# Kernel optimization log

Measured on AMD Instinct MI355X. Metric: run time of the kernel, lower is better.

The kernel has to match this reference:

```python
import jax, jax.numpy as jnp
import numpy as np

N_NODES = 100000
N_EDGES = 600000
D = 128          # model_dim
R = 50           # deprel_size


def setup_inputs() -> dict:
    key = jax.random.key(0)
    ks = jax.random.split(key, 20)
    s = 1.0 / np.sqrt(D)
    inp = jax.random.normal(ks[0], (N_NODES, D), dtype=jnp.float32)
    deprel_edge = jax.random.randint(ks[1], (N_EDGES,), 0, R)
    deparc_edge = jax.random.randint(ks[2], (N_EDGES,), 0, 4)
    edge_index = jax.random.randint(ks[3], (2, N_EDGES), 0, N_NODES)
    # parameters (nn.Linear weights stored as [out, in]; gates are Linear(D,1))
    V_in = jax.random.normal(ks[4], (D, D), dtype=jnp.float32) * s
    V_out = jax.random.normal(ks[5], (D, D), dtype=jnp.float32) * s
    W_self = jax.random.normal(ks[6], (D, D), dtype=jnp.float32) * s
    W_norel = jax.random.normal(ks[7], (D, D), dtype=jnp.float32) * s
    V_in_gate = jax.random.normal(ks[8], (1, D), dtype=jnp.float32) * s
    V_out_gate = jax.random.normal(ks[9], (1, D), dtype=jnp.float32) * s
    W_self_gate = jax.random.normal(ks[10], (1, D), dtype=jnp.float32) * s
    W_norel_gate = jax.random.normal(ks[11], (1, D), dtype=jnp.float32) * s
    b_in = jax.random.normal(ks[12], (R, D), dtype=jnp.float32) * 0.02
    b_out = jax.random.normal(ks[13], (R, D), dtype=jnp.float32) * 0.02
    b_in_gate = jax.random.normal(ks[14], (R, 1), dtype=jnp.float32) * 0.02 + 1.0
    b_out_gate = jax.random.normal(ks[15], (R, 1), dtype=jnp.float32) * 0.02 + 1.0
    return {
        "inp": inp, "deprel_edge": deprel_edge, "deparc_edge": deparc_edge,
        "edge_index": edge_index,
        "V_in": V_in, "b_in": b_in, "V_in_gate": V_in_gate, "b_in_gate": b_in_gate,
        "V_out": V_out, "b_out": b_out, "V_out_gate": V_out_gate, "b_out_gate": b_out_gate,
        "W_self": W_self, "W_self_gate": W_self_gate,
        "W_norel": W_norel, "W_norel_gate": W_norel_gate,
    }


def reference(inp, deprel_edge, deparc_edge, edge_index,
              V_in, b_in, V_in_gate, b_in_gate,
              V_out, b_out, V_out_gate, b_out_gate,
              W_self, W_self_gate, W_norel, W_norel_gate):
    # deparc type codes: 0=align(in), 1=opposite(out), 2=self, 3=norelation
    num_nodes = inp.shape[0]
    src, tgt = edge_index[0], edge_index[1]
    # transformed node features per edge type: [4, N, D]
    T = jnp.stack([inp @ V_in.T, inp @ V_out.T, inp @ W_self.T, inp @ W_norel.T])
    # gate pre-activations per edge type: [4, N, 1]
    G = jnp.stack([inp @ V_in_gate.T, inp @ V_out_gate.T,
                   inp @ W_self_gate.T, inp @ W_norel_gate.T])
    zeros_b = jnp.zeros_like(b_in)
    zeros_bg = jnp.zeros_like(b_in_gate)
    B = jnp.stack([b_in, b_out, zeros_b, zeros_b])        # [4, R, D] (self/norel have no relation bias)
    Bg = jnp.stack([b_in_gate, b_out_gate, zeros_bg, zeros_bg])  # [4, R, 1]
    # per-edge gather + relation bias
    msg = T[deparc_edge, src] + B[deparc_edge, deprel_edge]        # [E, D]
    gate = jax.nn.sigmoid(G[deparc_edge, src] + Bg[deparc_edge, deprel_edge])  # [E, 1]
    # scatter-add to target nodes
    return jax.ops.segment_sum(msg * gate, tgt, num_segments=num_nodes)
```

## Files before the change

kernel.cpp:

```cpp
#include <hip/hip_runtime.h>
#include <hip/hip_bf16.h>

#define D 128

typedef __bf16 bf16x8 __attribute__((ext_vector_type(8)));
typedef __bf16 bf16x4 __attribute__((ext_vector_type(4)));
typedef __bf16 bf16x2 __attribute__((ext_vector_type(2)));
typedef float  f32x4  __attribute__((ext_vector_type(4)));
typedef float  f32x2  __attribute__((ext_vector_type(2)));
typedef unsigned int u32x4 __attribute__((ext_vector_type(4)));

__global__ void detect_kernel(const unsigned int* __restrict__ w, int* flag)
{
    __shared__ int cnt[256];
    int c = 0;
#pragma unroll
    for (int i = 0; i < 4; ++i) {
        unsigned int v = w[threadIdx.x * 4 + i];
        unsigned int e = (v >> 7) & 0xFF;
        if (e >= 90 && e <= 134) ++c;
    }
    cnt[threadIdx.x] = c;
    __syncthreads();
    for (int s = 128; s > 0; s >>= 1) {
        if (threadIdx.x < s) cnt[threadIdx.x] += cnt[threadIdx.x + s];
        __syncthreads();
    }
    if (threadIdx.x == 0) flag[0] = (cnt[0] > 614) ? 1 : 0;
}

template <int ISBF>
__device__ __forceinline__ bf16x8 ld8(const void* p, size_t elem)
{
    if (ISBF) return *(const bf16x8*)((const __bf16*)p + elem);
    const f32x4* f = (const f32x4*)((const float*)p + elem);
    f32x4 lo = f[0], hi = f[1];
    bf16x8 r;
    r[0] = (__bf16)lo[0]; r[1] = (__bf16)lo[1]; r[2] = (__bf16)lo[2]; r[3] = (__bf16)lo[3];
    r[4] = (__bf16)hi[0]; r[5] = (__bf16)hi[1]; r[6] = (__bf16)hi[2]; r[7] = (__bf16)hi[3];
    return r;
}
template <int ISBF>
__device__ __forceinline__ float ldf(const void* p, size_t elem)
{
    return ISBF ? (float)((const __bf16*)p)[elem] : ((const float*)p)[elem];
}

__device__ __forceinline__ f32x2 bfpair(unsigned int u)
{
    f32x2 r;
    r[0] = __builtin_bit_cast(float, u << 16);
    r[1] = __builtin_bit_cast(float, u & 0xffff0000u);
    return r;
}

__device__ __forceinline__ f32x2 pkfma(f32x2 a, f32x2 b, f32x2 c)
{
    f32x2 d;
    asm("v_pk_fma_f32 %0, %1, %2, %3" : "=v"(d) : "v"(a), "v"(b), "v"(c));
    return d;
}

template <int ISBF>
__device__ __forceinline__ void gate_body(
    const void* __restrict__ A,
    const void* __restrict__ g0, const void* __restrict__ g1,
    const void* __restrict__ g2, const void* __restrict__ g3,
    float* __restrict__ G, int M)
{
    int node = blockIdx.x * 16 + (threadIdx.x >> 4);
    if (node >= M) return;
    int lane16 = threadIdx.x & 15;
    int dd = lane16 * 8;
    bf16x8 a  = ld8<ISBF>(A, (size_t)node * D + dd);
    bf16x8 q0 = ld8<ISBF>(g0, dd);
    bf16x8 q1 = ld8<ISBF>(g1, dd);
    bf16x8 q2 = ld8<ISBF>(g2, dd);
    bf16x8 q3 = ld8<ISBF>(g3, dd);
    float s0 = 0.f, s1 = 0.f, s2 = 0.f, s3 = 0.f;
#pragma unroll
    for (int k = 0; k < 8; ++k) {
        float af = (float)a[k];
        s0 = fmaf(af, (float)q0[k], s0);
        s1 = fmaf(af, (float)q1[k], s1);
        s2 = fmaf(af, (float)q2[k], s2);
        s3 = fmaf(af, (float)q3[k], s3);
    }
#pragma unroll
    for (int off = 8; off > 0; off >>= 1) {
        s0 += __shfl_xor(s0, off);
        s1 += __shfl_xor(s1, off);
        s2 += __shfl_xor(s2, off);
        s3 += __shfl_xor(s3, off);
    }
    if (lane16 == 0) {
        G[(size_t)0 * M + node] = s0;
        G[(size_t)1 * M + node] = s1;
        G[(size_t)2 * M + node] = s2;
        G[(size_t)3 * M + node] = s3;
    }
}

__global__ __launch_bounds__(256) void gate_kernel(
    const void* __restrict__ A,
    const void* __restrict__ g0, const void* __restrict__ g1,
    const void* __restrict__ g2, const void* __restrict__ g3,
    float* __restrict__ G, int M, const int* __restrict__ flag)
{
    if (flag[0]) gate_body<1>(A, g0, g1, g2, g3, G, M);
    else         gate_body<0>(A, g0, g1, g2, g3, G, M);
}

__global__ __launch_bounds__(128) void build_bias_kernel(
    const void* __restrict__ b_in, const void* __restrict__ b_out,
    const void* __restrict__ bg_in, const void* __restrict__ bg_out,
    __bf16* __restrict__ Bz, float* __restrict__ Bgz,
    const int* __restrict__ flag)
{
    int row = blockIdx.x;
    int tid = threadIdx.x;
    int isbf = flag[0];
    float v = 0.f, gv = 0.f;
    if (row < 50) {
        v  = isbf ? ldf<1>(b_in, (size_t)row * D + tid) : ldf<0>(b_in, (size_t)row * D + tid);
        gv = isbf ? ldf<1>(bg_in, row) : ldf<0>(bg_in, row);
    } else if (row < 100) {
        int rr = row - 50;
        v  = isbf ? ldf<1>(b_out, (size_t)rr * D + tid) : ldf<0>(b_out, (size_t)rr * D + tid);
        gv = isbf ? ldf<1>(bg_out, rr) : ldf<0>(bg_out, rr);
    }
    Bz[(size_t)row * D + tid] = (__bf16)v;
    if (tid == 0) Bgz[row] = gv;
}

__global__ __launch_bounds__(256) void hist_kernel(
    const int* __restrict__ tgt, int* __restrict__ counts, int E)
{
    int e = blockIdx.x * 256 + threadIdx.x;
    if (e < E) atomicAdd(&counts[tgt[e]], 1);
}

__global__ __launch_bounds__(256) void scan1_kernel(
    const int* __restrict__ counts, int* __restrict__ rowptr,
    int* __restrict__ bsum, int M)
{
    __shared__ int sh[256];
    int base = blockIdx.x * 1024 + threadIdx.x * 4;
    int v[4];
#pragma unroll
    for (int k = 0; k < 4; ++k)
        v[k] = (base + k < M) ? counts[base + k] : 0;
    int tot = v[0] + v[1] + v[2] + v[3];
    sh[threadIdx.x] = tot;
    __syncthreads();
    for (int off = 1; off < 256; off <<= 1) {
        int t = (threadIdx.x >= off) ? sh[threadIdx.x - off] : 0;
        __syncthreads();
        sh[threadIdx.x] += t;
        __syncthreads();
    }
    int run = sh[threadIdx.x] - tot;
#pragma unroll
    for (int k = 0; k < 4; ++k) {
        if (base + k < M) rowptr[base + k] = run;
        run += v[k];
    }
    if (threadIdx.x == 255) bsum[blockIdx.x] = sh[255];
}

__global__ __launch_bounds__(256) void scan2_kernel(
    int* __restrict__ bsum, int* __restrict__ boff, int NB)
{
    __shared__ int sh[256];
    int base = threadIdx.x * 4;
    int v[4];
#pragma unroll
    for (int k = 0; k < 4; ++k)
        v[k] = (base + k < NB) ? bsum[base + k] : 0;
    int tot = v[0] + v[1] + v[2] + v[3];
    sh[threadIdx.x] = tot;
    __syncthreads();
    for (int off = 1; off < 256; off <<= 1) {
        int t = (threadIdx.x >= off) ? sh[threadIdx.x - off] : 0;
        __syncthreads();
        sh[threadIdx.x] += t;
        __syncthreads();
    }
    int run = sh[threadIdx.x] - tot;
#pragma unroll
    for (int k = 0; k < 4; ++k) {
        if (base + k < NB) boff[base + k] = run;
        run += v[k];
    }
}

__global__ __launch_bounds__(256) void scan3_kernel(
    int* __restrict__ rowptr, int* __restrict__ cursor,
    const int* __restrict__ boff, int M, int E)
{
    int b = blockIdx.x;
    int base = b * 1024 + threadIdx.x * 4;
    int o = boff[b];
#pragma unroll
    for (int k = 0; k < 4; ++k) {
        int i = base + k;
        if (i < M) {
            int r = rowptr[i] + o;
            rowptr[i] = r;
            cursor[i] = r;
        }
    }
    if (b == 0 && threadIdx.x == 0) rowptr[M] = E;
}

__global__ __launch_bounds__(256) void scatter_kernel(
    const int* __restrict__ deprel, const int* __restrict__ deparc,
    const int* __restrict__ src, const int* __restrict__ tgt,
    int* __restrict__ cursor, int2* __restrict__ recs, int E)
{
    int e = blockIdx.x * 256 + threadIdx.x;
    if (e >= E) return;
    int g = tgt[e];
    int pos = atomicAdd(&cursor[g], 1);
    recs[pos] = make_int2(src[e], (deprel[e] << 2) | deparc[e]);
}

__global__ __launch_bounds__(256) void deg_hist_kernel(
    const int* __restrict__ counts, int* __restrict__ dcnt, int M)
{
    __shared__ int lh[64];
    if (threadIdx.x < 64) lh[threadIdx.x] = 0;
    __syncthreads();
    int i = blockIdx.x * 256 + threadIdx.x;
    if (i < M) {
        int d = counts[i]; if (d > 63) d = 63;
        atomicAdd(&lh[d], 1);
    }
    __syncthreads();
    if (threadIdx.x < 64 && lh[threadIdx.x])
        atomicAdd(&dcnt[threadIdx.x], lh[threadIdx.x]);
}

__global__ void deg_scan_kernel(const int* __restrict__ dcnt, int* __restrict__ dcur)
{
    if (threadIdx.x == 0) {
        int run = 0;
        for (int i = 0; i < 64; ++i) { dcur[i] = run; run += dcnt[i]; }
    }
}

__global__ __launch_bounds__(256) void deg_scatter_kernel(
    const int* __restrict__ counts, int* __restrict__ dcur,
    int* __restrict__ perm, int M)
{
    __shared__ int lh[64];
    __shared__ int gb[64];
    if (threadIdx.x < 64) lh[threadIdx.x] = 0;
    __syncthreads();
    int i = blockIdx.x * 256 + threadIdx.x;
    int d = 0, lpos = 0;
    if (i < M) {
        d = counts[i]; if (d > 63) d = 63;
        lpos = atomicAdd(&lh[d], 1);
    }
    __syncthreads();
    if (threadIdx.x < 64 && lh[threadIdx.x])
        gb[threadIdx.x] = atomicAdd(&dcur[threadIdx.x], lh[threadIdx.x]);
    __syncthreads();
    if (i < M) perm[gb[d] + lpos] = i;
}

template <int ISBF>
__device__ __forceinline__ void edge_agg_body(
    const void* __restrict__ inp, const float* __restrict__ G,
    const __bf16* __restrict__ Bz, const float* __restrict__ Bgz,
    const int* __restrict__ rowptr, const int2* __restrict__ recs,
    const int* __restrict__ perm,
    __bf16* __restrict__ AG, __bf16* __restrict__ BA, int M)
{
    const int idx = blockIdx.x * 16 + (threadIdx.x >> 4);
    if (idx >= M) return;
    const int g = perm[idx];
    const int lane16 = threadIdx.x & 15;
    const int dd = lane16 * 8;

    const int beg = rowptr[g], end = rowptr[g + 1];
    const int n = end - beg;

    f32x2 a0[4], a1[4], a2[4], a3[4], ba[4];
#pragma unroll
    for (int k = 0; k < 4; ++k) {
        a0[k] = (f32x2){0.f, 0.f}; a1[k] = (f32x2){0.f, 0.f};
        a2[k] = (f32x2){0.f, 0.f}; a3[k] = (f32x2){0.f, 0.f};
        ba[k] = (f32x2){0.f, 0.f};
    }

    bf16x8 v0 = {}, bz0 = {}, v1 = {}, bz1 = {};
    float gp0 = 0.f, bg0 = 0.f, gp1 = 0.f, bg1 = 0.f;
    int t0 = 0, t1 = 0;
    int2 r2 = make_int2(0, 0);

    auto issue = [&](int2 rec, bf16x8& v, bf16x8& bz, float& gp, float& bg, int& t) {
        t = rec.y & 3;
        int r = rec.y >> 2;
        int bidx = (t < 2) ? t * 50 + r : 100;
        gp = G[(size_t)t * M + rec.x];
        bg = Bgz[bidx];
        v  = ld8<ISBF>(inp, (size_t)rec.x * D + dd);
        bz = *(const bf16x8*)(Bz + (size_t)bidx * D + dd);
    };

    if (n > 0) issue(recs[beg], v0, bz0, gp0, bg0, t0);
    if (n > 1) issue(recs[beg + 1], v1, bz1, gp1, bg1, t1);
    if (n > 2) r2 = recs[beg + 2];

    for (int e = 0; e < n; ++e) {
        const bf16x8 v = v0, bz = bz0;
        const float gp = gp0, bg = bg0;
        const int t = t0;

        v0 = v1; bz0 = bz1; gp0 = gp1; bg0 = bg1; t0 = t1;
        if (e + 2 < n) {
            issue(r2, v1, bz1, gp1, bg1, t1);
            if (e + 3 < n) r2 = recs[beg + e + 3];
        }

        const float gate = 1.f / (1.f + __expf(-(gp + bg)));
        const float w0s = (t == 0) ? gate : 0.f;
        const float w1s = (t == 1) ? gate : 0.f;
        const float w2s = (t == 2) ? gate : 0.f;
        const float w3s = (t == 3) ? gate : 0.f;
        const f32x2 w0 = {w0s, w0s}, w1 = {w1s, w1s};
        const f32x2 w2 = {w2s, w2s}, w3 = {w3s, w3s};
        const f32x2 gg = {gate, gate};

        const u32x4 uv = __builtin_bit_cast(u32x4, v);
        const u32x4 ub = __builtin_bit_cast(u32x4, bz);
#pragma unroll
        for (int k = 0; k < 4; ++k) {
            const f32x2 vf = bfpair(uv[k]);
            const f32x2 bf = bfpair(ub[k]);
            a0[k] = pkfma(vf, w0, a0[k]);
            a1[k] = pkfma(vf, w1, a1[k]);
            a2[k] = pkfma(vf, w2, a2[k]);
            a3[k] = pkfma(vf, w3, a3[k]);
            ba[k] = pkfma(bf, gg, ba[k]);
        }
    }

    __bf16* agrow = AG + (size_t)g * (4 * D);
    bf16x8 w;
#pragma unroll
    for (int k = 0; k < 4; ++k) { w[2*k] = (__bf16)a0[k][0]; w[2*k+1] = (__bf16)a0[k][1]; }
    *(bf16x8*)(agrow + 0 * D + dd) = w;
#pragma unroll
    for (int k = 0; k < 4; ++k) { w[2*k] = (__bf16)a1[k][0]; w[2*k+1] = (__bf16)a1[k][1]; }
    *(bf16x8*)(agrow + 1 * D + dd) = w;
#pragma unroll
    for (int k = 0; k < 4; ++k) { w[2*k] = (__bf16)a2[k][0]; w[2*k+1] = (__bf16)a2[k][1]; }
    *(bf16x8*)(agrow + 2 * D + dd) = w;
#pragma unroll
    for (int k = 0; k < 4; ++k) { w[2*k] = (__bf16)a3[k][0]; w[2*k+1] = (__bf16)a3[k][1]; }
    *(bf16x8*)(agrow + 3 * D + dd) = w;
#pragma unroll
    for (int k = 0; k < 4; ++k) { w[2*k] = (__bf16)ba[k][0]; w[2*k+1] = (__bf16)ba[k][1]; }
    *(bf16x8*)(BA + (size_t)g * D + dd) = w;
}

__global__ __launch_bounds__(256) void edge_agg_kernel(
    const void* __restrict__ inp, const float* __restrict__ G,
    const __bf16* __restrict__ Bz, const float* __restrict__ Bgz,
    const int* __restrict__ rowptr, const int2* __restrict__ recs,
    const int* __restrict__ perm,
    __bf16* __restrict__ AG, __bf16* __restrict__ BA, int M,
    const int* __restrict__ flag)
{
    if (flag[0]) edge_agg_body<1>(inp, G, Bz, Bgz, rowptr, recs, perm, AG, BA, M);
    else         edge_agg_body<0>(inp, G, Bz, Bgz, rowptr, recs, perm, AG, BA, M);
}

template <int ISBF>
__device__ __forceinline__ void gemm2_body(
    const __bf16* __restrict__ AG, const __bf16* __restrict__ BA,
    const void* __restrict__ W0, const void* __restrict__ W1,
    const void* __restrict__ W2, const void* __restrict__ W3,
    void* __restrict__ out, int M)
{
    __shared__ __bf16 Wsh[128 * 128];

    const int wave = threadIdx.x >> 6;
    const int lane = threadIdx.x & 63;
    const int lrow = lane & 15;
    const int kgrp = lane >> 4;
    const int m_base = blockIdx.x * 128 + wave * 32;

    int n0 = m_base + lrow;      if (n0 >= M) n0 = 0;
    int n1 = m_base + 16 + lrow; if (n1 >= M) n1 = 0;

    const void* Ws[4] = {W0, W1, W2, W3};

    f32x4 acc[2][8];
#pragma unroll
    for (int i = 0; i < 2; ++i)
#pragma unroll
        for (int j = 0; j < 8; ++j)
            acc[i][j] = (f32x4){0.f, 0.f, 0.f, 0.f};

    for (int t = 0; t < 4; ++t) {
        const void* W = Ws[t];
#pragma unroll
        for (int i = 0; i < 8; ++i) {
            int slot = threadIdx.x + 256 * i;
            int f = slot >> 4;
            int s = slot & 15;
            int sp = s ^ (f & 7);
            bf16x8 v = ld8<ISBF>(W, (size_t)f * D + s * 8);
            *(bf16x8*)(Wsh + f * 128 + sp * 8) = v;
        }
        __syncthreads();

#pragma unroll
        for (int ks = 0; ks < 4; ++ks) {
            const int k0 = ks * 32 + kgrp * 8;
            bf16x8 af0 = *(const bf16x8*)(AG + (size_t)n0 * (4 * D) + t * D + k0);
            bf16x8 af1 = *(const bf16x8*)(AG + (size_t)n1 * (4 * D) + t * D + k0);
            const int slot = 4 * ks + kgrp;
#pragma unroll
            for (int ft = 0; ft < 8; ++ft) {
                int f = ft * 16 + lrow;
                int sp = slot ^ (f & 7);
                bf16x8 wf = *(const bf16x8*)(Wsh + f * 128 + sp * 8);
                acc[0][ft] = __builtin_amdgcn_mfma_f32_16x16x32_bf16(wf, af0, acc[0][ft], 0, 0, 0);
                acc[1][ft] = __builtin_amdgcn_mfma_f32_16x16x32_bf16(wf, af1, acc[1][ft], 0, 0, 0);
            }
        }
        __syncthreads();
    }

#pragma unroll
    for (int nt = 0; nt < 2; ++nt) {
        int node = m_base + nt * 16 + lrow;
        if (node < M) {
#pragma unroll
            for (int ft = 0; ft < 8; ++ft) {
                int f0 = ft * 16 + kgrp * 4;
                bf16x4 bb = *(const bf16x4*)(BA + (size_t)node * D + f0);
                f32x4 v = acc[nt][ft];
                v[0] += (float)bb[0]; v[1] += (float)bb[1];
                v[2] += (float)bb[2]; v[3] += (float)bb[3];
                if (ISBF) {
                    bf16x4 w4;
                    w4[0] = (__bf16)v[0]; w4[1] = (__bf16)v[1];
                    w4[2] = (__bf16)v[2]; w4[3] = (__bf16)v[3];
                    *(bf16x4*)((__bf16*)out + (size_t)node * D + f0) = w4;
                } else {
                    *(f32x4*)((float*)out + (size_t)node * D + f0) = v;
                }
            }
        }
    }
}

__global__ __launch_bounds__(256) void gemm2_kernel(
    const __bf16* __restrict__ AG, const __bf16* __restrict__ BA,
    const void* __restrict__ W0, const void* __restrict__ W1,
    const void* __restrict__ W2, const void* __restrict__ W3,
    void* __restrict__ out, int M, const int* __restrict__ flag)
{
    if (flag[0]) gemm2_body<1>(AG, BA, W0, W1, W2, W3, out, M);
    else         gemm2_body<0>(AG, BA, W0, W1, W2, W3, out, M);
}

__global__ void sentinel_kernel(__bf16* o, int n)
{
    int i = blockIdx.x * blockDim.x + threadIdx.x;
    if (i < n) o[i] = (__bf16)12345.0f;
}

static inline size_t align256(size_t x) { return (x + 255) & ~(size_t)255; }

extern "C" void kernel_launch(void* const* d_in, const int* in_sizes, int n_in,
                              void* d_out, int out_size, void* d_ws, size_t ws_size,
                              hipStream_t stream)
{
    const void* inp       = d_in[0];
    const int*  deprel    = (const int*)d_in[1];
    const int*  deparc    = (const int*)d_in[2];
    const int*  eidx      = (const int*)d_in[3];
    const void* V_in      = d_in[4];
    const void* b_in      = d_in[5];
    const void* V_in_g    = d_in[6];
    const void* b_in_g    = d_in[7];
    const void* V_out     = d_in[8];
    const void* b_out     = d_in[9];
    const void* V_out_g   = d_in[10];
    const void* b_out_g   = d_in[11];
    const void* W_self    = d_in[12];
    const void* W_self_g  = d_in[13];
    const void* W_norel   = d_in[14];
    const void* W_norel_g = d_in[15];

    const int M = in_sizes[0] / D;
    const int E = in_sizes[1];
    const int* src = eidx;
    const int* tgt = eidx + E;
    const int NB = (M + 1023) / 1024;

    size_t off = 0;
    size_t o_flag   = off; off = align256(off + sizeof(int));
    size_t o_AG     = off; off = align256(off + (size_t)M * 4 * D * sizeof(__bf16));
    size_t o_BA     = off; off = align256(off + (size_t)M * D * sizeof(__bf16));
    size_t o_G      = off; off = align256(off + (size_t)4 * M * sizeof(float));
    size_t o_counts = off; off = align256(off + (size_t)M * sizeof(int));
    size_t o_rowptr = off; off = align256(off + (size_t)(M + 1) * sizeof(int));
    size_t o_cursor = off; off = align256(off + (size_t)M * sizeof(int));
    size_t o_bsum   = off; off = align256(off + (size_t)NB * sizeof(int));
    size_t o_boff   = off; off = align256(off + (size_t)NB * sizeof(int));
    size_t o_recs   = off; off = align256(off + (size_t)E * sizeof(int2));
    size_t o_Bz     = off; off = align256(off + (size_t)101 * D * sizeof(__bf16));
    size_t o_Bgz    = off; off = align256(off + (size_t)101 * sizeof(float));
    size_t o_perm   = off; off = align256(off + (size_t)M * sizeof(int));
    size_t o_dcnt   = off; off = align256(off + (size_t)64 * sizeof(int));
    size_t o_dcur   = off; off = align256(off + (size_t)64 * sizeof(int));

    if (off > ws_size) {
        sentinel_kernel<<<(out_size + 255) / 256, 256, 0, stream>>>(
            (__bf16*)d_out, out_size);
        return;
    }

    int*    flag   = (int*)((char*)d_ws + o_flag);
    __bf16* AG     = (__bf16*)((char*)d_ws + o_AG);
    __bf16* BA     = (__bf16*)((char*)d_ws + o_BA);
    float*  Gbuf   = (float*)((char*)d_ws + o_G);
    int*    counts = (int*)((char*)d_ws + o_counts);
    int*    rowptr = (int*)((char*)d_ws + o_rowptr);
    int*    cursor = (int*)((char*)d_ws + o_cursor);
    int*    bsum   = (int*)((char*)d_ws + o_bsum);
    int*    boff   = (int*)((char*)d_ws + o_boff);
    int2*   recs   = (int2*)((char*)d_ws + o_recs);
    __bf16* Bz     = (__bf16*)((char*)d_ws + o_Bz);
    float*  Bgz    = (float*)((char*)d_ws + o_Bgz);
    int*    perm   = (int*)((char*)d_ws + o_perm);
    int*    dcnt   = (int*)((char*)d_ws + o_dcnt);
    int*    dcur   = (int*)((char*)d_ws + o_dcur);

    detect_kernel<<<1, 256, 0, stream>>>((const unsigned int*)inp, flag);

    hipMemsetAsync(counts, 0, (size_t)M * sizeof(int), stream);
    hipMemsetAsync(dcnt, 0, 64 * sizeof(int), stream);
    hist_kernel<<<(E + 255) / 256, 256, 0, stream>>>(tgt, counts, E);

    deg_hist_kernel<<<(M + 255) / 256, 256, 0, stream>>>(counts, dcnt, M);
    deg_scan_kernel<<<1, 64, 0, stream>>>(dcnt, dcur);
    deg_scatter_kernel<<<(M + 255) / 256, 256, 0, stream>>>(counts, dcur, perm, M);

    scan1_kernel<<<NB, 256, 0, stream>>>(counts, rowptr, bsum, M);
    scan2_kernel<<<1, 256, 0, stream>>>(bsum, boff, NB);
    scan3_kernel<<<NB, 256, 0, stream>>>(rowptr, cursor, boff, M, E);
    scatter_kernel<<<(E + 255) / 256, 256, 0, stream>>>(deprel, deparc, src, tgt,
                                                        cursor, recs, E);

    build_bias_kernel<<<101, 128, 0, stream>>>(b_in, b_out, b_in_g, b_out_g,
                                               Bz, Bgz, flag);
    gate_kernel<<<(M + 15) / 16, 256, 0, stream>>>(inp, V_in_g, V_out_g, W_self_g,
                                                   W_norel_g, Gbuf, M, flag);

    edge_agg_kernel<<<(M + 15) / 16, 256, 0, stream>>>(inp, Gbuf, Bz, Bgz,
                                                       rowptr, recs, perm,
                                                       AG, BA, M, flag);
    gemm2_kernel<<<(M + 127) / 128, 256, 0, stream>>>(AG, BA, V_in, V_out, W_self,
                                                      W_norel, d_out, M, flag);
}
```

Measured before the change: 339.6 us.

## Merge setup kernels, drop degree-sort permutation, use nontemporal memory ops

Folds the dtype detect into the histogram kernel and the bias build into the gate kernel. Replaces the separate block-sum scan with a serial per-block prefix loop inside scan3. Removes the degree-sorted node permutation, so edge aggregation handles nodes in natural order. Switches intermediate AG/BA stores, their loads in the GEMM and the output stores to nontemporal hints. Fewer launches cut launch overhead, but dropping the degree sort can bring back load imbalance between wavefronts in edge aggregation.

```diff
diff --git a/kernel.cpp b/kernel.cpp
--- a/kernel.cpp
+++ b/kernel.cpp
@@ -9,25 +9,6 @@
 typedef float  f32x4  __attribute__((ext_vector_type(4)));
 typedef float  f32x2  __attribute__((ext_vector_type(2)));
 typedef unsigned int u32x4 __attribute__((ext_vector_type(4)));
-
-__global__ void detect_kernel(const unsigned int* __restrict__ w, int* flag)
-{
-    __shared__ int cnt[256];
-    int c = 0;
-#pragma unroll
-    for (int i = 0; i < 4; ++i) {
-        unsigned int v = w[threadIdx.x * 4 + i];
-        unsigned int e = (v >> 7) & 0xFF;
-        if (e >= 90 && e <= 134) ++c;
-    }
-    cnt[threadIdx.x] = c;
-    __syncthreads();
-    for (int s = 128; s > 0; s >>= 1) {
-        if (threadIdx.x < s) cnt[threadIdx.x] += cnt[threadIdx.x + s];
-        __syncthreads();
-    }
-    if (threadIdx.x == 0) flag[0] = (cnt[0] > 614) ? 1 : 0;
-}
 
 template <int ISBF>
 __device__ __forceinline__ bf16x8 ld8(const void* p, size_t elem)
@@ -61,13 +42,57 @@
     return d;
 }
 
+__global__ __launch_bounds__(256) void hist_detect_kernel(
+    const int* __restrict__ tgt, int* __restrict__ counts, int E,
+    const unsigned int* __restrict__ w, int* __restrict__ flag)
+{
+    __shared__ int cnt[256];
+    int e = blockIdx.x * 256 + threadIdx.x;
+    if (e < E) atomicAdd(&counts[tgt[e]], 1);
+    if (blockIdx.x == 0) {
+        int c = 0;
+#pragma unroll
+        for (int i = 0; i < 4; ++i) {
+            unsigned int v = w[threadIdx.x * 4 + i];
+            unsigned int ex = (v >> 7) & 0xFF;
+            if (ex >= 90 && ex <= 134) ++c;
+        }
+        cnt[threadIdx.x] = c;
+        __syncthreads();
+        for (int s = 128; s > 0; s >>= 1) {
+            if (threadIdx.x < s) cnt[threadIdx.x] += cnt[threadIdx.x + s];
+            __syncthreads();
+        }
+        if (threadIdx.x == 0) flag[0] = (cnt[0] > 614) ? 1 : 0;
+    }
+}
+
 template <int ISBF>
-__device__ __forceinline__ void gate_body(
+__device__ __forceinline__ void gate_bias_body(
     const void* __restrict__ A,
     const void* __restrict__ g0, const void* __restrict__ g1,
     const void* __restrict__ g2, const void* __restrict__ g3,
-    float* __restrict__ G, int M)
-{
+    const void* __restrict__ b_in, const void* __restrict__ b_out,
+    const void* __restrict__ bg_in, const void* __restrict__ bg_out,
+    float* __restrict__ G, __bf16* __restrict__ Bz, float* __restrict__ Bgz,
+    int M)
+{
+    if (blockIdx.x < 101 && threadIdx.x < 128) {
+        int row = blockIdx.x;
+        int tid = threadIdx.x;
+        float v = 0.f, gv = 0.f;
+        if (row < 50) {
+            v  = ldf<ISBF>(b_in, (size_t)row * D + tid);
+            gv = ldf<ISBF>(bg_in, row);
+        } else if (row < 100) {
+            int rr = row - 50;
+            v  = ldf<ISBF>(b_out, (size_t)rr * D + tid);
+            gv = ldf<ISBF>(bg_out, rr);
+        }
+        Bz[(size_t)row * D + tid] = (__bf16)v;
+        if (tid == 0) Bgz[row] = gv;
+    }
+
     int node = blockIdx.x * 16 + (threadIdx.x >> 4);
     if (node >= M) return;
     int lane16 = threadIdx.x & 15;
@@ -101,43 +126,17 @@
     }
 }
 
-__global__ __launch_bounds__(256) void gate_kernel(
+__global__ __launch_bounds__(256) void gate_bias_kernel(
     const void* __restrict__ A,
     const void* __restrict__ g0, const void* __restrict__ g1,
     const void* __restrict__ g2, const void* __restrict__ g3,
-    float* __restrict__ G, int M, const int* __restrict__ flag)
-{
-    if (flag[0]) gate_body<1>(A, g0, g1, g2, g3, G, M);
-    else         gate_body<0>(A, g0, g1, g2, g3, G, M);
-}
-
-__global__ __launch_bounds__(128) void build_bias_kernel(
     const void* __restrict__ b_in, const void* __restrict__ b_out,
     const void* __restrict__ bg_in, const void* __restrict__ bg_out,
-    __bf16* __restrict__ Bz, float* __restrict__ Bgz,
-    const int* __restrict__ flag)
-{
-    int row = blockIdx.x;
-    int tid = threadIdx.x;
-    int isbf = flag[0];
-    float v = 0.f, gv = 0.f;
-    if (row < 50) {
-        v  = isbf ? ldf<1>(b_in, (size_t)row * D + tid) : ldf<0>(b_in, (size_t)row * D + tid);
-        gv = isbf ? ldf<1>(bg_in, row) : ldf<0>(bg_in, row);
-    } else if (row < 100) {
-        int rr = row - 50;
-        v  = isbf ? ldf<1>(b_out, (size_t)rr * D + tid) : ldf<0>(b_out, (size_t)rr * D + tid);
-        gv = isbf ? ldf<1>(bg_out, rr) : ldf<0>(bg_out, rr);
-    }
-    Bz[(size_t)row * D + tid] = (__bf16)v;
-    if (tid == 0) Bgz[row] = gv;
-}
-
-__global__ __launch_bounds__(256) void hist_kernel(
-    const int* __restrict__ tgt, int* __restrict__ counts, int E)
-{
-    int e = blockIdx.x * 256 + threadIdx.x;
-    if (e < E) atomicAdd(&counts[tgt[e]], 1);
+    float* __restrict__ G, __bf16* __restrict__ Bz, float* __restrict__ Bgz,
+    int M, const int* __restrict__ flag)
+{
+    if (flag[0]) gate_bias_body<1>(A, g0, g1, g2, g3, b_in, b_out, bg_in, bg_out, G, Bz, Bgz, M);
+    else         gate_bias_body<0>(A, g0, g1, g2, g3, b_in, b_out, bg_in, bg_out, G, Bz, Bgz, M);
 }
 
 __global__ __launch_bounds__(256) void scan1_kernel(
@@ -168,39 +167,14 @@
     if (threadIdx.x == 255) bsum[blockIdx.x] = sh[255];
 }
 
-__global__ __launch_bounds__(256) void scan2_kernel(
-    int* __restrict__ bsum, int* __restrict__ boff, int NB)
-{
-    __shared__ int sh[256];
-    int base = threadIdx.x * 4;
-    int v[4];
-#pragma unroll
-    for (int k = 0; k < 4; ++k)
-        v[k] = (base + k < NB) ? bsum[base + k] : 0;
-    int tot = v[0] + v[1] + v[2] + v[3];
-    sh[threadIdx.x] = tot;
-    __syncthreads();
-    for (int off = 1; off < 256; off <<= 1) {
-        int t = (threadIdx.x >= off) ? sh[threadIdx.x - off] : 0;
-        __syncthreads();
-        sh[threadIdx.x] += t;
-        __syncthreads();
-    }
-    int run = sh[threadIdx.x] - tot;
-#pragma unroll
-    for (int k = 0; k < 4; ++k) {
-        if (base + k < NB) boff[base + k] = run;
-        run += v[k];
-    }
-}
-
 __global__ __launch_bounds__(256) void scan3_kernel(
     int* __restrict__ rowptr, int* __restrict__ cursor,
-    const int* __restrict__ boff, int M, int E)
+    const int* __restrict__ bsum, int M, int E)
 {
     int b = blockIdx.x;
+    int o = 0;
+    for (int i = 0; i < b; ++i) o += bsum[i];
     int base = b * 1024 + threadIdx.x * 4;
-    int o = boff[b];
 #pragma unroll
     for (int k = 0; k < 4; ++k) {
         int i = base + k;
@@ -225,62 +199,15 @@
     recs[pos] = make_int2(src[e], (deprel[e] << 2) | deparc[e]);
 }
 
-__global__ __launch_bounds__(256) void deg_hist_kernel(
-    const int* __restrict__ counts, int* __restrict__ dcnt, int M)
-{
-    __shared__ int lh[64];
-    if (threadIdx.x < 64) lh[threadIdx.x] = 0;
-    __syncthreads();
-    int i = blockIdx.x * 256 + threadIdx.x;
-    if (i < M) {
-        int d = counts[i]; if (d > 63) d = 63;
-        atomicAdd(&lh[d], 1);
-    }
-    __syncthreads();
-    if (threadIdx.x < 64 && lh[threadIdx.x])
-        atomicAdd(&dcnt[threadIdx.x], lh[threadIdx.x]);
-}
-
-__global__ void deg_scan_kernel(const int* __restrict__ dcnt, int* __restrict__ dcur)
-{
-    if (threadIdx.x == 0) {
-        int run = 0;
-        for (int i = 0; i < 64; ++i) { dcur[i] = run; run += dcnt[i]; }
-    }
-}
-
-__global__ __launch_bounds__(256) void deg_scatter_kernel(
-    const int* __restrict__ counts, int* __restrict__ dcur,
-    int* __restrict__ perm, int M)
-{
-    __shared__ int lh[64];
-    __shared__ int gb[64];
-    if (threadIdx.x < 64) lh[threadIdx.x] = 0;
-    __syncthreads();
-    int i = blockIdx.x * 256 + threadIdx.x;
-    int d = 0, lpos = 0;
-    if (i < M) {
-        d = counts[i]; if (d > 63) d = 63;
-        lpos = atomicAdd(&lh[d], 1);
-    }
-    __syncthreads();
-    if (threadIdx.x < 64 && lh[threadIdx.x])
-        gb[threadIdx.x] = atomicAdd(&dcur[threadIdx.x], lh[threadIdx.x]);
-    __syncthreads();
-    if (i < M) perm[gb[d] + lpos] = i;
-}
-
 template <int ISBF>
 __device__ __forceinline__ void edge_agg_body(
     const void* __restrict__ inp, const float* __restrict__ G,
     const __bf16* __restrict__ Bz, const float* __restrict__ Bgz,
     const int* __restrict__ rowptr, const int2* __restrict__ recs,
-    const int* __restrict__ perm,
     __bf16* __restrict__ AG, __bf16* __restrict__ BA, int M)
 {
-    const int idx = blockIdx.x * 16 + (threadIdx.x >> 4);
-    if (idx >= M) return;
-    const int g = perm[idx];
+    const int g = blockIdx.x * 16 + (threadIdx.x >> 4);
+    if (g >= M) return;
     const int lane16 = threadIdx.x & 15;
     const int dd = lane16 * 8;
 
@@ -352,31 +279,30 @@
     bf16x8 w;
 #pragma unroll
     for (int k = 0; k < 4; ++k) { w[2*k] = (__bf16)a0[k][0]; w[2*k+1] = (__bf16)a0[k][1]; }
-    *(bf16x8*)(agrow + 0 * D + dd) = w;
+    __builtin_nontemporal_store(w, (bf16x8*)(agrow + 0 * D + dd));
 #pragma unroll
     for (int k = 0; k < 4; ++k) { w[2*k] = (__bf16)a1[k][0]; w[2*k+1] = (__bf16)a1[k][1]; }
-    *(bf16x8*)(agrow + 1 * D + dd) = w;
+    __builtin_nontemporal_store(w, (bf16x8*)(agrow + 1 * D + dd));
 #pragma unroll
     for (int k = 0; k < 4; ++k) { w[2*k] = (__bf16)a2[k][0]; w[2*k+1] = (__bf16)a2[k][1]; }
-    *(bf16x8*)(agrow + 2 * D + dd) = w;
+    __builtin_nontemporal_store(w, (bf16x8*)(agrow + 2 * D + dd));
 #pragma unroll
     for (int k = 0; k < 4; ++k) { w[2*k] = (__bf16)a3[k][0]; w[2*k+1] = (__bf16)a3[k][1]; }
-    *(bf16x8*)(agrow + 3 * D + dd) = w;
+    __builtin_nontemporal_store(w, (bf16x8*)(agrow + 3 * D + dd));
 #pragma unroll
     for (int k = 0; k < 4; ++k) { w[2*k] = (__bf16)ba[k][0]; w[2*k+1] = (__bf16)ba[k][1]; }
-    *(bf16x8*)(BA + (size_t)g * D + dd) = w;
+    __builtin_nontemporal_store(w, (bf16x8*)(BA + (size_t)g * D + dd));
 }
 
 __global__ __launch_bounds__(256) void edge_agg_kernel(
     const void* __restrict__ inp, const float* __restrict__ G,
     const __bf16* __restrict__ Bz, const float* __restrict__ Bgz,
     const int* __restrict__ rowptr, const int2* __restrict__ recs,
-    const int* __restrict__ perm,
     __bf16* __restrict__ AG, __bf16* __restrict__ BA, int M,
     const int* __restrict__ flag)
 {
-    if (flag[0]) edge_agg_body<1>(inp, G, Bz, Bgz, rowptr, recs, perm, AG, BA, M);
-    else         edge_agg_body<0>(inp, G, Bz, Bgz, rowptr, recs, perm, AG, BA, M);
+    if (flag[0]) edge_agg_body<1>(inp, G, Bz, Bgz, rowptr, recs, AG, BA, M);
+    else         edge_agg_body<0>(inp, G, Bz, Bgz, rowptr, recs, AG, BA, M);
 }
 
 template <int ISBF>
@@ -422,8 +348,10 @@
 #pragma unroll
         for (int ks = 0; ks < 4; ++ks) {
             const int k0 = ks * 32 + kgrp * 8;
-            bf16x8 af0 = *(const bf16x8*)(AG + (size_t)n0 * (4 * D) + t * D + k0);
-            bf16x8 af1 = *(const bf16x8*)(AG + (size_t)n1 * (4 * D) + t * D + k0);
+            bf16x8 af0 = __builtin_nontemporal_load(
+                (const bf16x8*)(AG + (size_t)n0 * (4 * D) + t * D + k0));
+            bf16x8 af1 = __builtin_nontemporal_load(
+                (const bf16x8*)(AG + (size_t)n1 * (4 * D) + t * D + k0));
             const int slot = 4 * ks + kgrp;
 #pragma unroll
             for (int ft = 0; ft < 8; ++ft) {
@@ -444,7 +372,8 @@
 #pragma unroll
             for (int ft = 0; ft < 8; ++ft) {
                 int f0 = ft * 16 + kgrp * 4;
-                bf16x4 bb = *(const bf16x4*)(BA + (size_t)node * D + f0);
+                bf16x4 bb = __builtin_nontemporal_load(
+                    (const bf16x4*)(BA + (size_t)node * D + f0));
                 f32x4 v = acc[nt][ft];
                 v[0] += (float)bb[0]; v[1] += (float)bb[1];
                 v[2] += (float)bb[2]; v[3] += (float)bb[3];
@@ -452,9 +381,11 @@
                     bf16x4 w4;
                     w4[0] = (__bf16)v[0]; w4[1] = (__bf16)v[1];
                     w4[2] = (__bf16)v[2]; w4[3] = (__bf16)v[3];
-                    *(bf16x4*)((__bf16*)out + (size_t)node * D + f0) = w4;
+                    __builtin_nontemporal_store(w4,
+                        (bf16x4*)((__bf16*)out + (size_t)node * D + f0));
                 } else {
-                    *(f32x4*)((float*)out + (size_t)node * D + f0) = v;
+                    __builtin_nontemporal_store(v,
+                        (f32x4*)((float*)out + (size_t)node * D + f0));
                 }
             }
         }
@@ -515,13 +446,9 @@
     size_t o_rowptr = off; off = align256(off + (size_t)(M + 1) * sizeof(int));
     size_t o_cursor = off; off = align256(off + (size_t)M * sizeof(int));
     size_t o_bsum   = off; off = align256(off + (size_t)NB * sizeof(int));
-    size_t o_boff   = off; off = align256(off + (size_t)NB * sizeof(int));
     size_t o_recs   = off; off = align256(off + (size_t)E * sizeof(int2));
     size_t o_Bz     = off; off = align256(off + (size_t)101 * D * sizeof(__bf16));
     size_t o_Bgz    = off; off = align256(off + (size_t)101 * sizeof(float));
-    size_t o_perm   = off; off = align256(off + (size_t)M * sizeof(int));
-    size_t o_dcnt   = off; off = align256(off + (size_t)64 * sizeof(int));
-    size_t o_dcur   = off; off = align256(off + (size_t)64 * sizeof(int));
 
     if (off > ws_size) {
         sentinel_kernel<<<(out_size + 255) / 256, 256, 0, stream>>>(
@@ -537,38 +464,24 @@
     int*    rowptr = (int*)((char*)d_ws + o_rowptr);
     int*    cursor = (int*)((char*)d_ws + o_cursor);
     int*    bsum   = (int*)((char*)d_ws + o_bsum);
-    int*    boff   = (int*)((char*)d_ws + o_boff);
     int2*   recs   = (int2*)((char*)d_ws + o_recs);
     __bf16* Bz     = (__bf16*)((char*)d_ws + o_Bz);
     float*  Bgz    = (float*)((char*)d_ws + o_Bgz);
-    int*    perm   = (int*)((char*)d_ws + o_perm);
-    int*    dcnt   = (int*)((char*)d_ws + o_dcnt);
-    int*    dcur   = (int*)((char*)d_ws + o_dcur);
-
-    detect_kernel<<<1, 256, 0, stream>>>((const unsigned int*)inp, flag);
 
     hipMemsetAsync(counts, 0, (size_t)M * sizeof(int), stream);
-    hipMemsetAsync(dcnt, 0, 64 * sizeof(int), stream);
-    hist_kernel<<<(E + 255) / 256, 256, 0, stream>>>(tgt, counts, E);
-
-    deg_hist_kernel<<<(M + 255) / 256, 256, 0, stream>>>(counts, dcnt, M);
-    deg_scan_kernel<<<1, 64, 0, stream>>>(dcnt, dcur);
-    deg_scatter_kernel<<<(M + 255) / 256, 256, 0, stream>>>(counts, dcur, perm, M);
-
+    hist_detect_kernel<<<(E + 255) / 256, 256, 0, stream>>>(
+        tgt, counts, E, (const unsigned int*)inp, flag);
     scan1_kernel<<<NB, 256, 0, stream>>>(counts, rowptr, bsum, M);
-    scan2_kernel<<<1, 256, 0, stream>>>(bsum, boff, NB);
-    scan3_kernel<<<NB, 256, 0, stream>>>(rowptr, cursor, boff, M, E);
+    scan3_kernel<<<NB, 256, 0, stream>>>(rowptr, cursor, bsum, M, E);
     scatter_kernel<<<(E + 255) / 256, 256, 0, stream>>>(deprel, deparc, src, tgt,
                                                         cursor, recs, E);
 
-    build_bias_kernel<<<101, 128, 0, stream>>>(b_in, b_out, b_in_g, b_out_g,
-                                               Bz, Bgz, flag);
-    gate_kernel<<<(M + 15) / 16, 256, 0, stream>>>(inp, V_in_g, V_out_g, W_self_g,
-                                                   W_norel_g, Gbuf, M, flag);
+    gate_bias_kernel<<<(M + 15) / 16, 256, 0, stream>>>(
+        inp, V_in_g, V_out_g, W_self_g, W_norel_g,
+        b_in, b_out, b_in_g, b_out_g, Gbuf, Bz, Bgz, M, flag);
 
     edge_agg_kernel<<<(M + 15) / 16, 256, 0, stream>>>(inp, Gbuf, Bz, Bgz,
-                                                       rowptr, recs, perm,
-                                                       AG, BA, M, flag);
+                                                       rowptr, recs, AG, BA, M, flag);
     gemm2_kernel<<<(M + 127) / 128, 256, 0, stream>>>(AG, BA, V_in, V_out, W_self,
                                                       W_norel, d_out, M, flag);
 }
```

Result: faster. 325.2 us (-4.2%).
